# Optimization experiments

Hardware: AMD Instinct MI355X
Metric: run time of the kernel (lower is better)

The kernel has to match this reference:

```python
import jax, jax.numpy as jnp
from jax import lax
import numpy as np


def conv2d(x, w, pad):
    # x: NCHW, w: OIHW
    return lax.conv_general_dilated(x, w, (1, 1), [(pad, pad), (pad, pad)],
                                    dimension_numbers=("NCHW", "OIHW", "NCHW"))


def make_dct_dict(num_atoms, num_dims):
    i = np.arange(num_atoms)[:, None].astype(np.float64)
    n = np.arange(num_dims)[None, :].astype(np.float64)
    w = np.cos((2.0 * n + 1.0) * i * (np.pi / (2.0 * num_dims)))
    w = w / np.linalg.norm(w, axis=1, keepdims=True)
    return jnp.asarray(w.T, dtype=jnp.float32)  # [num_dims, num_atoms]


def setup_inputs() -> dict:
    key = jax.random.key(0)
    B, C, H, W = 8, 64, 64, 64      # C = num_dims
    A = 256                          # num_atoms
    ks = jax.random.split(key, 10)
    s = 0.05
    Dict = make_dct_dict(A, C)       # [C, A]
    L = jnp.sum(Dict ** 2)           # ||Dict||_F^2 (scalar parameter)
    return {
        "x": jax.random.normal(ks[0], (B, C, H, W), jnp.float32),
        "conv_w": jax.random.normal(ks[1], (A, C, 3, 3), jnp.float32) * s,
        "conv_b": jax.random.normal(ks[2], (A,), jnp.float32) * s,
        "res1_w1": jax.random.normal(ks[3], (A // 2, A, 3, 3), jnp.float32) * s,
        "res1_w2": jax.random.normal(ks[4], (A, A // 2, 1, 1), jnp.float32) * s,
        "res2_w1": jax.random.normal(ks[5], (A // 2, A, 3, 3), jnp.float32) * s,
        "res2_w2": jax.random.normal(ks[6], (A, A // 2, 1, 1), jnp.float32) * s,
        "ca_w1": jax.random.normal(ks[7], (A // 16, A), jnp.float32) * s,  # Linear(A, A//16)
        "ca_w2": jax.random.normal(ks[8], (A, A // 16), jnp.float32) * s,  # Linear(A//16, A)
        "sa_w": jax.random.normal(ks[9], (1, 2, 3, 3), jnp.float32) * s,
        "Dict": Dict,
        "L": L,
        "num_iters": 16,
    }


def reference(x, conv_w, conv_b, res1_w1, res1_w2, res2_w1, res2_w2,
              ca_w1, ca_w2, sa_w, Dict, L, num_iters):
    def res_block(h, w1, w2):
        t = conv2d(jax.nn.relu(h), w1, 1)
        t = conv2d(jax.nn.relu(t), w2, 0)
        return h + t

    l = conv2d(x, conv_w, 1) + conv_b[None, :, None, None]
    l = res_block(l, res1_w1, res1_w2)
    l = res_block(l, res2_w1, res2_w2)

    # CBAM: channel attention (shared MLP on avg/max pooled features)
    avg = jnp.mean(l, axis=(2, 3))  # [B, A]
    mx = jnp.max(l, axis=(2, 3))
    fc = lambda v: jax.nn.relu(v @ ca_w1.T) @ ca_w2.T
    l = l * jax.nn.sigmoid(fc(avg) + fc(mx))[:, :, None, None]
    # CBAM: spatial attention
    s2 = jnp.concatenate([jnp.mean(l, axis=1, keepdims=True),
                          jnp.max(l, axis=1, keepdims=True)], axis=1)  # [B,2,H,W]
    l = l * jax.nn.sigmoid(conv2d(s2, sa_w, 1))

    lam = jnp.transpose(l / L, (0, 2, 3, 1))   # [B,H,W,A] per-position thresholds
    xp = jnp.transpose(x, (0, 2, 3, 1))        # [B,H,W,C]

    A = Dict.shape[1]
    S = (jnp.eye(A, dtype=Dict.dtype) - (Dict.T @ Dict) / L).T  # [A,A]
    y = xp @ Dict                               # [B,H,W,A]
    yL = y / L

    soft = lambda v: jnp.sign(v) * jnp.maximum(jnp.abs(v) - lam, 0.0)

    z0 = soft(y)

    def step(z, _):
        return soft(z @ S + yL), None

    z, _ = lax.scan(step, z0, None, length=num_iters)
    x_recon = z @ Dict.T                        # [B,H,W,C]

    return (jnp.transpose(z, (0, 3, 1, 2)),
            jnp.transpose(x_recon, (0, 3, 1, 2)),
            Dict)
```

## Files before the change

### kernel.cpp

```cpp
#include <hip/hip_runtime.h>
#include <hip/hip_bf16.h>

typedef __attribute__((ext_vector_type(8))) short short8v;
typedef __attribute__((ext_vector_type(4))) short short4v;
typedef __attribute__((ext_vector_type(4))) float float4v;

__device__ __forceinline__ unsigned short f2bu(float v){
  __hip_bfloat16 h = __float2bfloat16(v);
  union { __hip_bfloat16 h; unsigned short u; } cv; cv.h = h; return cv.u;
}

__device__ __forceinline__ float softt(float v, float lam){
  float t = fabsf(v) - lam;
  float sg = (v > 0.f) ? 1.f : ((v < 0.f) ? -1.f : 0.f);
  return (t > 0.f) ? sg * t : 0.f;
}

__global__ void k_Lin(const float* __restrict__ Lsrc, float* __restrict__ Lb){
  Lb[0] = Lsrc[0];
}

__global__ void k_gram(const float* __restrict__ D, unsigned short* __restrict__ Gb){
  int j = blockIdx.x, a = threadIdx.x;
  float acc = 0.f;
  for (int c = 0; c < 64; ++c)
    acc += D[c*256 + j] * D[c*256 + a];
  Gb[j*256 + a] = f2bu(acc);
}

__global__ void k_transpD(const float* __restrict__ D, float* __restrict__ DT,
                          unsigned short* __restrict__ DTb){
  int gid = blockIdx.x * 256 + threadIdx.x;
  if (gid < 16384) {
    int a = gid >> 6, c = gid & 63;
    float v = D[c*256 + a];
    DT[gid] = v;
    DTb[gid] = f2bu(v);
  }
}

__global__ void k_castw(const float* __restrict__ w, unsigned short* __restrict__ wb,
                        int n){
  int gid = blockIdx.x * 256 + threadIdx.x;
  if (gid < n) wb[gid] = f2bu(w[gid]);
}

__global__ void k_permw3(const float* __restrict__ w, unsigned short* __restrict__ wb,
                         int logI, int n){
  int gid = blockIdx.x * 256 + threadIdx.x;
  if (gid >= n) return;
  int I = 1 << logI;
  int i = gid & (I - 1);
  int t = gid >> logI;
  int o = t / 9;
  int r = t - o * 9;
  wb[gid] = f2bu(w[((o << logI) + i) * 9 + r]);
}

template<int KS, int CIN, bool BIAS, bool RES, bool WF32, bool WBF>
__global__ __launch_bounds__(256) void k_conv(
    const unsigned short* __restrict__ in, const unsigned short* __restrict__ wb,
    const float* __restrict__ bias, const float* res, float* outf,
    unsigned short* __restrict__ outb, int Cout)
{
  constexpr int NCH  = CIN / 32;
  constexpr int LNCH = (NCH == 2) ? 1 : (NCH == 4 ? 2 : 3);
  constexpr int K    = KS * KS * CIN;

  __shared__ unsigned short Asb[32][40];
  __shared__ unsigned short Bsb[128][40];

  const int tid = threadIdx.x;
  int bx = blockIdx.x;
  { const int cpx = gridDim.x >> 3; bx = (bx & 7) * cpx + (bx >> 3); }
  const int m0  = bx * 32;
  const int n0  = blockIdx.y * 128;
  const int b   = m0 >> 12;
  const int hw0 = m0 & 4095;
  const int h   = hw0 >> 6;
  const int w0  = hw0 & 63;

  const int sm  = tid & 31;
  const int sq4 = tid >> 5;
  const int bn  = tid & 127;
  const int bq  = tid >> 7;

  const int w   = tid >> 6;
  const int ln  = tid & 63;
  const int q   = ln >> 4;
  const int l16 = ln & 15;

  float4v acc[2][2];
  #pragma unroll
  for (int nt = 0; nt < 2; ++nt)
    #pragma unroll
    for (int mt = 0; mt < 2; ++mt)
      acc[nt][mt] = (float4v){0.f, 0.f, 0.f, 0.f};

  int sA = 0, sB = NCH;
  if (KS == 3) { sA = (h == 0 ? 3 : 0) * NCH; sB = (h == 63 ? 6 : 9) * NCH; }

  short4v a_r;
  short8v b_r0, b_r1;

  auto pref = [&](int s){
    const int r    = s >> LNCH;
    const int ccid = s & (NCH - 1);
    int hh = h, ww = w0 + sm;
    bool ok = true;
    if (KS == 3) {
      const int dh = r / 3 - 1;
      const int dw = r - (r / 3) * 3 - 1;
      hh += dh; ww += dw;
      ok = ((unsigned)ww < 64u);
    }
    a_r = (short4v){0, 0, 0, 0};
    if (ok) {
      const unsigned short* ap = in +
          (((size_t)(b * CIN + ccid * 32 + sq4 * 4)) << 12) + (hh << 6) + ww;
      #pragma unroll
      for (int j = 0; j < 4; ++j)
        a_r[j] = (short)ap[(size_t)j << 12];
    }
    const unsigned short* bp = wb + (size_t)(n0 + bn) * K + s * 32 + bq * 16;
    b_r0 = *(const short8v*)(bp);
    b_r1 = *(const short8v*)(bp + 8);
  };

  pref(sA);
  for (int s = sA; s < sB; ) {
    *(short4v*)(&Asb[sm][sq4 * 4])      = a_r;
    *(short8v*)(&Bsb[bn][bq * 16])      = b_r0;
    *(short8v*)(&Bsb[bn][bq * 16 + 8])  = b_r1;
    __syncthreads();
    const int sn = s + 1;
    if (sn < sB) pref(sn);
    short8v Af[2];
    #pragma unroll
    for (int mt = 0; mt < 2; ++mt)
      Af[mt] = *(const short8v*)(&Asb[mt * 16 + l16][q * 8]);
    #pragma unroll
    for (int nt = 0; nt < 2; ++nt) {
      short8v Bf = *(const short8v*)(&Bsb[w * 32 + nt * 16 + l16][q * 8]);
      #pragma unroll
      for (int mt = 0; mt < 2; ++mt)
        acc[nt][mt] = __builtin_amdgcn_mfma_f32_16x16x32_bf16(
            Af[mt], Bf, acc[nt][mt], 0, 0, 0);
    }
    __syncthreads();
    s = sn;
  }

  #pragma unroll
  for (int nt = 0; nt < 2; ++nt) {
    const int n = n0 + w * 32 + nt * 16 + l16;
    float bv = 0.f;
    if (BIAS) bv = bias[n];
    #pragma unroll
    for (int mt = 0; mt < 2; ++mt) {
      const size_t base = (((size_t)(b * Cout + n)) << 12) + hw0 + mt * 16 + q * 4;
      float o[4];
      #pragma unroll
      for (int r2 = 0; r2 < 4; ++r2) o[r2] = acc[nt][mt][r2] + bv;
      if (RES) {
        float4 r4 = *(const float4*)(res + base);
        o[0] += r4.x; o[1] += r4.y; o[2] += r4.z; o[3] += r4.w;
      }
      if (WF32) {
        float4 o4; o4.x = o[0]; o4.y = o[1]; o4.z = o[2]; o4.w = o[3];
        *(float4*)(outf + base) = o4;
      }
      if (WBF) {
        short4v s4;
        #pragma unroll
        for (int r2 = 0; r2 < 4; ++r2) s4[r2] = (short)f2bu(fmaxf(o[r2], 0.f));
        *(short4v*)(outb + base) = s4;
      }
    }
  }
}

__global__ void k_pool(const float* __restrict__ l, float* __restrict__ avg,
                       float* __restrict__ mx){
  int b = blockIdx.y, a = blockIdx.x, tid = threadIdx.x;
  const float* p = l + ((size_t)(b * 256 + a) << 12);
  float s = 0.f, m = -1e30f;
  for (int i = tid; i < 4096; i += 256) { float v = p[i]; s += v; m = fmaxf(m, v); }
  __shared__ float ss[256], sm[256];
  ss[tid] = s; sm[tid] = m; __syncthreads();
  for (int o = 128; o > 0; o >>= 1) {
    if (tid < o) { ss[tid] += ss[tid+o]; sm[tid] = fmaxf(sm[tid], sm[tid+o]); }
    __syncthreads();
  }
  if (tid == 0) { avg[b*256+a] = ss[0] * (1.f/4096.f); mx[b*256+a] = sm[0]; }
}

__global__ void k_ca(const float* __restrict__ avg, const float* __restrict__ mx,
                     const float* __restrict__ w1, const float* __restrict__ w2,
                     float* __restrict__ cscale){
  int b = blockIdx.x, tid = threadIdx.x;
  __shared__ float h[16];
  if (tid < 16) {
    float sa = 0.f, sm = 0.f;
    for (int a = 0; a < 256; ++a) {
      float w = w1[tid*256 + a];
      sa += avg[b*256 + a] * w;
      sm += mx[b*256 + a] * w;
    }
    h[tid] = fmaxf(sa, 0.f) + fmaxf(sm, 0.f);
  }
  __syncthreads();
  float s = 0.f;
  for (int j = 0; j < 16; ++j) s += h[j] * w2[tid*16 + j];
  cscale[b*256 + tid] = 1.f / (1.f + __expf(-s));
}

__global__ void k_s2(const float* __restrict__ l, const float* __restrict__ cscale,
                     float* __restrict__ s2){
  int b = blockIdx.y;
  int hw = blockIdx.x * 256 + threadIdx.x;
  const float* p  = l + (((size_t)b * 256) << 12) + hw;
  const float* cs = cscale + b * 256;
  float s = 0.f, m = -1e30f;
  for (int a = 0; a < 256; ++a) {
    float v = p[(size_t)a << 12] * cs[a];
    s += v; m = fmaxf(m, v);
  }
  s2[((b*2) << 12) + hw]   = s * (1.f/256.f);
  s2[((b*2+1) << 12) + hw] = m;
}

__global__ void k_sa(const float* __restrict__ s2, const float* __restrict__ w,
                     float* __restrict__ sa){
  int b = blockIdx.y;
  int hw = blockIdx.x * 256 + threadIdx.x;
  int h = hw >> 6, ww = hw & 63;
  float acc = 0.f;
  for (int ch = 0; ch < 2; ++ch)
    for (int dh = -1; dh <= 1; ++dh)
      for (int dw = -1; dw <= 1; ++dw) {
        int hh = h + dh, wc = ww + dw;
        if ((unsigned)hh < 64u && (unsigned)wc < 64u)
          acc += s2[((b*2+ch) << 12) + (hh << 6) + wc] * w[ch*9 + (dh+1)*3 + (dw+1)];
      }
  sa[(b << 12) + hw] = 1.f / (1.f + __expf(-acc));
}

#define XTS 80

__device__ __forceinline__ int zswz(int row, int col){
  return row * 256 + ((((col >> 3) ^ (row & 7)) << 3) | (col & 7));
}

__global__ __launch_bounds__(512, 2) void k_lista(
    const float* __restrict__ x,
    const unsigned short* __restrict__ DTb,
    const unsigned short* __restrict__ Gb,
    const float* __restrict__ lmap, const float* __restrict__ csc,
    const float* __restrict__ sav, const float* __restrict__ Lb,
    float* __restrict__ zout)
{
  __shared__ unsigned short xTb[32][XTS];
  __shared__ unsigned short zbuf[2][32 * 256];

  const int tid = threadIdx.x;
  const int m0  = blockIdx.x * 32;
  const int b   = m0 >> 12;
  const int hw0 = m0 & 4095;
  const float invL = 1.0f / Lb[0];

  {
    const int i  = tid & 31;
    const int c0 = tid >> 5;
    #pragma unroll
    for (int cc = 0; cc < 4; ++cc) {
      int c = c0 + cc * 16;
      xTb[i][c] = f2bu(x[((b * 64 + c) << 12) + hw0 + i]);
    }
  }
  __syncthreads();

  const int w   = tid >> 6;
  const int ln  = tid & 63;
  const int q   = ln >> 4;
  const int l16 = ln & 15;

  float z[4][4], yl[4][4], lamr[4][4];

  #pragma unroll
  for (int ct = 0; ct < 2; ++ct) {
    const int col = w * 32 + ct * 16 + l16;
    const short8v B0 = *(const short8v*)(DTb + col * 64 + q * 8);
    const short8v B1 = *(const short8v*)(DTb + col * 64 + 32 + q * 8);
    const float cscv = csc[b * 256 + col];
    #pragma unroll
    for (int rt = 0; rt < 2; ++rt) {
      float4v a = {0.f, 0.f, 0.f, 0.f};
      const short8v A0 = *(const short8v*)(&xTb[rt * 16 + l16][q * 8]);
      const short8v A1 = *(const short8v*)(&xTb[rt * 16 + l16][32 + q * 8]);
      a = __builtin_amdgcn_mfma_f32_16x16x32_bf16(A0, B0, a, 0, 0, 0);
      a = __builtin_amdgcn_mfma_f32_16x16x32_bf16(A1, B1, a, 0, 0, 0);
      const int t = ct * 2 + rt;
      #pragma unroll
      for (int r = 0; r < 4; ++r) {
        const int row = rt * 16 + q * 4 + r;
        const float lv = lmap[(((size_t)(b * 256 + col)) << 12) + hw0 + row];
        const float sv = sav[(b << 12) + hw0 + row];
        const float lm = ((lv * cscv) * sv) * invL;
        const float yv = a[r];
        lamr[t][r] = lm;
        yl[t][r]   = yv * invL;
        const float z0 = softt(yv, lm);
        z[t][r] = z0;
        zbuf[0][zswz(row, col)] = f2bu(z0);
      }
    }
  }

  short8v Bg[2][8];
  #pragma unroll
  for (int ct = 0; ct < 2; ++ct)
    #pragma unroll
    for (int ks = 0; ks < 8; ++ks)
      Bg[ct][ks] = *(const short8v*)(
          Gb + (size_t)(w * 32 + ct * 16 + l16) * 256 + ks * 32 + q * 8);

  __syncthreads();

  const int rx = l16 & 7;
  int cur = 0;
  for (int it = 0; it < 16; ++it) {
    float4v acc[2][2];
    #pragma unroll
    for (int ct = 0; ct < 2; ++ct)
      #pragma unroll
      for (int rt = 0; rt < 2; ++rt)
        acc[ct][rt] = (float4v){0.f, 0.f, 0.f, 0.f};

    #pragma unroll
    for (int rt = 0; rt < 2; ++rt) {
      const unsigned short* zrow = &zbuf[cur][(rt * 16 + l16) * 256];
      #pragma unroll
      for (int ks = 0; ks < 8; ++ks) {
        const short8v A = *(const short8v*)(zrow + (((ks * 4 + q) ^ rx) << 3));
        acc[0][rt] = __builtin_amdgcn_mfma_f32_16x16x32_bf16(A, Bg[0][ks], acc[0][rt], 0, 0, 0);
        acc[1][rt] = __builtin_amdgcn_mfma_f32_16x16x32_bf16(A, Bg[1][ks], acc[1][rt], 0, 0, 0);
      }
    }
    #pragma unroll
    for (int ct = 0; ct < 2; ++ct) {
      const int col = w * 32 + ct * 16 + l16;
      #pragma unroll
      for (int rt = 0; rt < 2; ++rt) {
        const int t = ct * 2 + rt;
        #pragma unroll
        for (int r = 0; r < 4; ++r) {
          const int row = rt * 16 + q * 4 + r;
          const float nz = softt(z[t][r] + yl[t][r] - acc[ct][rt][r] * invL,
                                 lamr[t][r]);
          z[t][r] = nz;
          zbuf[cur ^ 1][zswz(row, col)] = f2bu(nz);
        }
      }
    }
    __syncthreads();
    cur ^= 1;
  }

  #pragma unroll
  for (int ct = 0; ct < 2; ++ct) {
    const int col = w * 32 + ct * 16 + l16;
    #pragma unroll
    for (int rt = 0; rt < 2; ++rt) {
      const int t = ct * 2 + rt;
      #pragma unroll
      for (int r = 0; r < 4; ++r) {
        const int row = rt * 16 + q * 4 + r;
        zout[(size_t)(m0 + row) * 256 + col] = z[t][r];
      }
    }
  }
}

__global__ __launch_bounds__(256) void k_recon_simple(
    const float* __restrict__ z, const float* __restrict__ DT,
    float* __restrict__ out1)
{
  __shared__ float zs[16][256];
  const int tid = threadIdx.x;
  const int r0  = blockIdx.x * 16;
  const int b   = r0 >> 12;
  const int hw0 = r0 & 4095;

  for (int idx = tid; idx < 4096; idx += 256) {
    int r = idx >> 8, k = idx & 255;
    zs[r][k] = z[(r0 + r) * 256 + k];
  }
  __syncthreads();

  const int c  = tid & 63;
  const int rg = tid >> 6;
  float acc[4] = {0.f, 0.f, 0.f, 0.f};
  for (int a = 0; a < 256; ++a) {
    float d = DT[a * 64 + c];
    #pragma unroll
    for (int i = 0; i < 4; ++i) acc[i] += zs[rg + 4*i][a] * d;
  }
  #pragma unroll
  for (int i = 0; i < 4; ++i) {
    int r = rg + 4*i;
    out1[((b * 64 + c) << 12) + hw0 + r] = acc[i];
  }
}

__global__ __launch_bounds__(256) void k_zout_t(const float* __restrict__ z,
                                                float* __restrict__ out0){
  __shared__ float zs[64][65];
  const int tid = threadIdx.x;
  const int hwt = blockIdx.x * 64;
  const int at  = blockIdx.y * 64;
  const int b   = blockIdx.z;
  const int j   = tid & 63;
  const int i0  = tid >> 6;
  #pragma unroll
  for (int k = 0; k < 16; ++k) {
    int i = i0 + k * 4;
    zs[i][j] = z[(size_t)(b * 4096 + hwt + i) * 256 + at + j];
  }
  __syncthreads();
  #pragma unroll
  for (int k = 0; k < 16; ++k) {
    int i = i0 + k * 4;
    out0[(((size_t)(b * 256 + at + i)) << 12) + hwt + j] = zs[j][i];
  }
}

__global__ void k_dictout_f32(const float* __restrict__ D, float* __restrict__ out2){
  int i = blockIdx.x * 256 + threadIdx.x;
  if (i < 16384) out2[i] = D[i];
}

extern "C" void kernel_launch(void* const* d_in, const int* in_sizes, int n_in,
                              void* d_out, int out_size, void* d_ws, size_t ws_size,
                              hipStream_t stream)
{
  (void)in_sizes; (void)n_in; (void)out_size; (void)ws_size;

  const float* x    = (const float*)d_in[0];
  const float* cw   = (const float*)d_in[1];
  const float* cb   = (const float*)d_in[2];
  const float* r1w1 = (const float*)d_in[3];
  const float* r1w2 = (const float*)d_in[4];
  const float* r2w1 = (const float*)d_in[5];
  const float* r2w2 = (const float*)d_in[6];
  const float* caw1 = (const float*)d_in[7];
  const float* caw2 = (const float*)d_in[8];
  const float* saw  = (const float*)d_in[9];
  const float* D    = (const float*)d_in[10];
  const float* Lsrc = (const float*)d_in[11];

  float* p = (float*)d_ws;
  float* DT   = p; p += 16384;
  float* Lb   = p; p += 8;
  unsigned short* Gb  = (unsigned short*)p; p += 32768;
  unsigned short* DTb = (unsigned short*)p; p += 8192;
  unsigned short* cwb   = (unsigned short*)p; p += 73728;
  unsigned short* r1w1b = (unsigned short*)p; p += 147456;
  unsigned short* r1w2b = (unsigned short*)p; p += 16384;
  unsigned short* r2w1b = (unsigned short*)p; p += 147456;
  unsigned short* r2w2b = (unsigned short*)p; p += 16384;
  float* avg  = p; p += 2048;
  float* mx   = p; p += 2048;
  float* csc  = p; p += 2048;
  float* s2   = p; p += 65536;
  float* sa   = p; p += 32768;
  float* l    = p; p += 8388608;
  float* scr  = p; p += 8388608;
  float* zt   = p; p += 8388608;
  float* z    = zt;

  unsigned short* xb = (unsigned short*)scr;
  unsigned short* lb = (unsigned short*)(scr + 1048576);
  unsigned short* tb = (unsigned short*)(scr + 1048576 + 4194304);

  float* out0 = (float*)d_out;
  float* out1 = out0 + (size_t)8*256*4096;
  float* out2 = out1 + (size_t)8*64*4096;

  dim3 b256(256);

  k_Lin<<<dim3(1), dim3(1), 0, stream>>>(Lsrc, Lb);
  k_gram<<<dim3(256), b256, 0, stream>>>(D, Gb);
  k_transpD<<<dim3(64), b256, 0, stream>>>(D, DT, DTb);
  k_permw3<<<dim3(576),  b256, 0, stream>>>(cw,   cwb,   6, 147456);
  k_permw3<<<dim3(1152), b256, 0, stream>>>(r1w1, r1w1b, 8, 294912);
  k_castw <<<dim3(128),  b256, 0, stream>>>(r1w2, r1w2b, 32768);
  k_permw3<<<dim3(1152), b256, 0, stream>>>(r2w1, r2w1b, 8, 294912);
  k_castw <<<dim3(128),  b256, 0, stream>>>(r2w2, r2w2b, 32768);
  k_castw <<<dim3(8192), b256, 0, stream>>>(x, xb, 2097152);

  k_conv<3,  64, true,  false, true,  true ><<<dim3(1024, 2), b256, 0, stream>>>(
      xb, cwb, cb, (const float*)nullptr, l, lb, 256);
  k_conv<3, 256, false, false, false, true ><<<dim3(1024, 1), b256, 0, stream>>>(
      lb, r1w1b, (const float*)nullptr, (const float*)nullptr, (float*)nullptr, tb, 128);
  k_conv<1, 128, false, true,  true,  true ><<<dim3(1024, 2), b256, 0, stream>>>(
      tb, r1w2b, (const float*)nullptr, l, l, lb, 256);
  k_conv<3, 256, false, false, false, true ><<<dim3(1024, 1), b256, 0, stream>>>(
      lb, r2w1b, (const float*)nullptr, (const float*)nullptr, (float*)nullptr, tb, 128);
  k_conv<1, 128, false, true,  true,  false><<<dim3(1024, 2), b256, 0, stream>>>(
      tb, r2w2b, (const float*)nullptr, l, l, (unsigned short*)nullptr, 256);

  k_pool<<<dim3(256, 8), b256, 0, stream>>>(l, avg, mx);
  k_ca<<<dim3(8), b256, 0, stream>>>(avg, mx, caw1, caw2, csc);
  k_s2<<<dim3(16, 8), b256, 0, stream>>>(l, csc, s2);
  k_sa<<<dim3(16, 8), b256, 0, stream>>>(s2, saw, sa);

  k_lista<<<dim3(1024), dim3(512), 0, stream>>>(x, DTb, Gb, l, csc, sa, Lb, z);

  k_recon_simple<<<dim3(2048), b256, 0, stream>>>(z, DT, out1);
  k_zout_t<<<dim3(64, 4, 8), b256, 0, stream>>>(z, out0);
  k_dictout_f32<<<dim3(64), b256, 0, stream>>>(D, out2);
}
```

Baseline: 579.8 us.

## Enlarge conv M-tile to 64 pixels and transpose LISTA MFMA operand roles

The conv kernel now covers 64 output pixels per block instead of 32, with 4 M-subtiles per wave. This halves the grid and reuses each loaded weight tile across twice as many pixels, at the cost of more accumulator registers. The LISTA kernel swaps MFMA operands so the Gram matrix is the A operand and z is B. That lets each lane hold 4 consecutive atoms, so z is written to LDS as packed short4 stores and to global memory as float4 stores instead of scalar ones. The soft-threshold is also rewritten branch-free with copysign, and the occupancy hint on LISTA is dropped.

After: 489.1 us. -15.7%, faster.

```diff
diff --git a/kernel.cpp b/kernel.cpp
--- a/kernel.cpp
+++ b/kernel.cpp
@@ -11,9 +11,9 @@
 }
 
 __device__ __forceinline__ float softt(float v, float lam){
-  float t = fabsf(v) - lam;
-  float sg = (v > 0.f) ? 1.f : ((v < 0.f) ? -1.f : 0.f);
-  return (t > 0.f) ? sg * t : 0.f;
+  float t = fmaxf(fabsf(v) - lam, 0.f);
+  float r = copysignf(t, v);
+  return (v == 0.f) ? 0.f : r;
 }
 
 __global__ void k_Lin(const float* __restrict__ Lsrc, float* __restrict__ Lb){
@@ -67,21 +67,21 @@
   constexpr int LNCH = (NCH == 2) ? 1 : (NCH == 4 ? 2 : 3);
   constexpr int K    = KS * KS * CIN;
 
-  __shared__ unsigned short Asb[32][40];
+  __shared__ unsigned short Asb[64][40];
   __shared__ unsigned short Bsb[128][40];
 
   const int tid = threadIdx.x;
   int bx = blockIdx.x;
   { const int cpx = gridDim.x >> 3; bx = (bx & 7) * cpx + (bx >> 3); }
-  const int m0  = bx * 32;
+  const int m0  = bx * 64;
   const int n0  = blockIdx.y * 128;
   const int b   = m0 >> 12;
   const int hw0 = m0 & 4095;
   const int h   = hw0 >> 6;
   const int w0  = hw0 & 63;
 
-  const int sm  = tid & 31;
-  const int sq4 = tid >> 5;
+  const int sm  = tid & 63;
+  const int sq8 = tid >> 6;
   const int bn  = tid & 127;
   const int bq  = tid >> 7;
 
@@ -90,17 +90,17 @@
   const int q   = ln >> 4;
   const int l16 = ln & 15;
 
-  float4v acc[2][2];
+  float4v acc[2][4];
   #pragma unroll
   for (int nt = 0; nt < 2; ++nt)
     #pragma unroll
-    for (int mt = 0; mt < 2; ++mt)
+    for (int mt = 0; mt < 4; ++mt)
       acc[nt][mt] = (float4v){0.f, 0.f, 0.f, 0.f};
 
   int sA = 0, sB = NCH;
   if (KS == 3) { sA = (h == 0 ? 3 : 0) * NCH; sB = (h == 63 ? 6 : 9) * NCH; }
 
-  short4v a_r;
+  short8v a_r;
   short8v b_r0, b_r1;
 
   auto pref = [&](int s){
@@ -114,12 +114,12 @@
       hh += dh; ww += dw;
       ok = ((unsigned)ww < 64u);
     }
-    a_r = (short4v){0, 0, 0, 0};
+    a_r = (short8v){0,0,0,0,0,0,0,0};
     if (ok) {
       const unsigned short* ap = in +
-          (((size_t)(b * CIN + ccid * 32 + sq4 * 4)) << 12) + (hh << 6) + ww;
-      #pragma unroll
-      for (int j = 0; j < 4; ++j)
+          (((size_t)(b * CIN + ccid * 32 + sq8 * 8)) << 12) + (hh << 6) + ww;
+      #pragma unroll
+      for (int j = 0; j < 8; ++j)
         a_r[j] = (short)ap[(size_t)j << 12];
     }
     const unsigned short* bp = wb + (size_t)(n0 + bn) * K + s * 32 + bq * 16;
@@ -129,21 +129,21 @@
 
   pref(sA);
   for (int s = sA; s < sB; ) {
-    *(short4v*)(&Asb[sm][sq4 * 4])      = a_r;
+    *(short8v*)(&Asb[sm][sq8 * 8])      = a_r;
     *(short8v*)(&Bsb[bn][bq * 16])      = b_r0;
     *(short8v*)(&Bsb[bn][bq * 16 + 8])  = b_r1;
     __syncthreads();
     const int sn = s + 1;
     if (sn < sB) pref(sn);
-    short8v Af[2];
-    #pragma unroll
-    for (int mt = 0; mt < 2; ++mt)
+    short8v Af[4];
+    #pragma unroll
+    for (int mt = 0; mt < 4; ++mt)
       Af[mt] = *(const short8v*)(&Asb[mt * 16 + l16][q * 8]);
     #pragma unroll
     for (int nt = 0; nt < 2; ++nt) {
       short8v Bf = *(const short8v*)(&Bsb[w * 32 + nt * 16 + l16][q * 8]);
       #pragma unroll
-      for (int mt = 0; mt < 2; ++mt)
+      for (int mt = 0; mt < 4; ++mt)
         acc[nt][mt] = __builtin_amdgcn_mfma_f32_16x16x32_bf16(
             Af[mt], Bf, acc[nt][mt], 0, 0, 0);
     }
@@ -157,7 +157,7 @@
     float bv = 0.f;
     if (BIAS) bv = bias[n];
     #pragma unroll
-    for (int mt = 0; mt < 2; ++mt) {
+    for (int mt = 0; mt < 4; ++mt) {
       const size_t base = (((size_t)(b * Cout + n)) << 12) + hw0 + mt * 16 + q * 4;
       float o[4];
       #pragma unroll
@@ -248,11 +248,7 @@
 
 #define XTS 80
 
-__device__ __forceinline__ int zswz(int row, int col){
-  return row * 256 + ((((col >> 3) ^ (row & 7)) << 3) | (col & 7));
-}
-
-__global__ __launch_bounds__(512, 2) void k_lista(
+__global__ __launch_bounds__(512) void k_lista(
     const float* __restrict__ x,
     const unsigned short* __restrict__ DTb,
     const unsigned short* __restrict__ Gb,
@@ -284,83 +280,87 @@
   const int ln  = tid & 63;
   const int q   = ln >> 4;
   const int l16 = ln & 15;
+  const int rx  = l16 & 7;
 
   float z[4][4], yl[4][4], lamr[4][4];
 
-  #pragma unroll
-  for (int ct = 0; ct < 2; ++ct) {
-    const int col = w * 32 + ct * 16 + l16;
-    const short8v B0 = *(const short8v*)(DTb + col * 64 + q * 8);
-    const short8v B1 = *(const short8v*)(DTb + col * 64 + 32 + q * 8);
-    const float cscv = csc[b * 256 + col];
-    #pragma unroll
-    for (int rt = 0; rt < 2; ++rt) {
+  short8v Sg[2][8];
+  #pragma unroll
+  for (int at = 0; at < 2; ++at)
+    #pragma unroll
+    for (int ks = 0; ks < 8; ++ks)
+      Sg[at][ks] = *(const short8v*)(
+          Gb + (size_t)(w * 32 + at * 16 + l16) * 256 + ks * 32 + q * 8);
+
+  #pragma unroll
+  for (int at = 0; at < 2; ++at) {
+    const short8v A0 = *(const short8v*)(DTb + (w*32 + at*16 + l16) * 64 + q * 8);
+    const short8v A1 = *(const short8v*)(DTb + (w*32 + at*16 + l16) * 64 + 32 + q * 8);
+    const int chunk = ((w * 4 + at * 2 + (q >> 1)) ^ rx);
+    #pragma unroll
+    for (int pt = 0; pt < 2; ++pt) {
       float4v a = {0.f, 0.f, 0.f, 0.f};
-      const short8v A0 = *(const short8v*)(&xTb[rt * 16 + l16][q * 8]);
-      const short8v A1 = *(const short8v*)(&xTb[rt * 16 + l16][32 + q * 8]);
+      const short8v B0 = *(const short8v*)(&xTb[pt * 16 + l16][q * 8]);
+      const short8v B1 = *(const short8v*)(&xTb[pt * 16 + l16][32 + q * 8]);
       a = __builtin_amdgcn_mfma_f32_16x16x32_bf16(A0, B0, a, 0, 0, 0);
       a = __builtin_amdgcn_mfma_f32_16x16x32_bf16(A1, B1, a, 0, 0, 0);
-      const int t = ct * 2 + rt;
+      const int t = at * 2 + pt;
+      const int p = pt * 16 + l16;
+      short4v pk;
       #pragma unroll
       for (int r = 0; r < 4; ++r) {
-        const int row = rt * 16 + q * 4 + r;
-        const float lv = lmap[(((size_t)(b * 256 + col)) << 12) + hw0 + row];
-        const float sv = sav[(b << 12) + hw0 + row];
-        const float lm = ((lv * cscv) * sv) * invL;
+        const int atom = w * 32 + at * 16 + q * 4 + r;
+        const float lv = lmap[(((size_t)(b * 256 + atom)) << 12) + hw0 + p];
+        const float sv = sav[(b << 12) + hw0 + p];
+        const float cv = csc[b * 256 + atom];
+        const float lm = ((lv * cv) * sv) * invL;
         const float yv = a[r];
         lamr[t][r] = lm;
         yl[t][r]   = yv * invL;
         const float z0 = softt(yv, lm);
         z[t][r] = z0;
-        zbuf[0][zswz(row, col)] = f2bu(z0);
-      }
-    }
-  }
-
-  short8v Bg[2][8];
-  #pragma unroll
-  for (int ct = 0; ct < 2; ++ct)
-    #pragma unroll
-    for (int ks = 0; ks < 8; ++ks)
-      Bg[ct][ks] = *(const short8v*)(
-          Gb + (size_t)(w * 32 + ct * 16 + l16) * 256 + ks * 32 + q * 8);
-
+        pk[r] = (short)f2bu(z0);
+      }
+      *(short4v*)(&zbuf[0][p * 256 + (chunk << 3) + (q & 1) * 4]) = pk;
+    }
+  }
   __syncthreads();
 
-  const int rx = l16 & 7;
   int cur = 0;
   for (int it = 0; it < 16; ++it) {
     float4v acc[2][2];
     #pragma unroll
-    for (int ct = 0; ct < 2; ++ct)
-      #pragma unroll
-      for (int rt = 0; rt < 2; ++rt)
-        acc[ct][rt] = (float4v){0.f, 0.f, 0.f, 0.f};
-
-    #pragma unroll
-    for (int rt = 0; rt < 2; ++rt) {
-      const unsigned short* zrow = &zbuf[cur][(rt * 16 + l16) * 256];
+    for (int at = 0; at < 2; ++at)
+      #pragma unroll
+      for (int pt = 0; pt < 2; ++pt)
+        acc[at][pt] = (float4v){0.f, 0.f, 0.f, 0.f};
+
+    #pragma unroll
+    for (int pt = 0; pt < 2; ++pt) {
+      const unsigned short* zrow = &zbuf[cur][(pt * 16 + l16) * 256];
       #pragma unroll
       for (int ks = 0; ks < 8; ++ks) {
-        const short8v A = *(const short8v*)(zrow + (((ks * 4 + q) ^ rx) << 3));
-        acc[0][rt] = __builtin_amdgcn_mfma_f32_16x16x32_bf16(A, Bg[0][ks], acc[0][rt], 0, 0, 0);
-        acc[1][rt] = __builtin_amdgcn_mfma_f32_16x16x32_bf16(A, Bg[1][ks], acc[1][rt], 0, 0, 0);
-      }
-    }
-    #pragma unroll
-    for (int ct = 0; ct < 2; ++ct) {
-      const int col = w * 32 + ct * 16 + l16;
-      #pragma unroll
-      for (int rt = 0; rt < 2; ++rt) {
-        const int t = ct * 2 + rt;
+        const short8v B = *(const short8v*)(zrow + (((ks * 4 + q) ^ rx) << 3));
+        acc[0][pt] = __builtin_amdgcn_mfma_f32_16x16x32_bf16(Sg[0][ks], B, acc[0][pt], 0, 0, 0);
+        acc[1][pt] = __builtin_amdgcn_mfma_f32_16x16x32_bf16(Sg[1][ks], B, acc[1][pt], 0, 0, 0);
+      }
+    }
+    #pragma unroll
+    for (int at = 0; at < 2; ++at) {
+      const int chunk = ((w * 4 + at * 2 + (q >> 1)) ^ rx);
+      #pragma unroll
+      for (int pt = 0; pt < 2; ++pt) {
+        const int t = at * 2 + pt;
+        const int p = pt * 16 + l16;
+        short4v pk;
         #pragma unroll
         for (int r = 0; r < 4; ++r) {
-          const int row = rt * 16 + q * 4 + r;
-          const float nz = softt(z[t][r] + yl[t][r] - acc[ct][rt][r] * invL,
+          const float nz = softt(z[t][r] + yl[t][r] - acc[at][pt][r] * invL,
                                  lamr[t][r]);
           z[t][r] = nz;
-          zbuf[cur ^ 1][zswz(row, col)] = f2bu(nz);
+          pk[r] = (short)f2bu(nz);
         }
+        *(short4v*)(&zbuf[cur ^ 1][p * 256 + (chunk << 3) + (q & 1) * 4]) = pk;
       }
     }
     __syncthreads();
@@ -368,16 +368,14 @@
   }
 
   #pragma unroll
-  for (int ct = 0; ct < 2; ++ct) {
-    const int col = w * 32 + ct * 16 + l16;
-    #pragma unroll
-    for (int rt = 0; rt < 2; ++rt) {
-      const int t = ct * 2 + rt;
-      #pragma unroll
-      for (int r = 0; r < 4; ++r) {
-        const int row = rt * 16 + q * 4 + r;
-        zout[(size_t)(m0 + row) * 256 + col] = z[t][r];
-      }
+  for (int at = 0; at < 2; ++at) {
+    #pragma unroll
+    for (int pt = 0; pt < 2; ++pt) {
+      const int t = at * 2 + pt;
+      const int p = pt * 16 + l16;
+      float4 o;
+      o.x = z[t][0]; o.y = z[t][1]; o.z = z[t][2]; o.w = z[t][3];
+      *(float4*)(&zout[(size_t)(m0 + p) * 256 + w * 32 + at * 16 + q * 4]) = o;
     }
   }
 }
@@ -499,15 +497,15 @@
   k_castw <<<dim3(128),  b256, 0, stream>>>(r2w2, r2w2b, 32768);
   k_castw <<<dim3(8192), b256, 0, stream>>>(x, xb, 2097152);
 
-  k_conv<3,  64, true,  false, true,  true ><<<dim3(1024, 2), b256, 0, stream>>>(
+  k_conv<3,  64, true,  false, true,  true ><<<dim3(512, 2), b256, 0, stream>>>(
       xb, cwb, cb, (const float*)nullptr, l, lb, 256);
-  k_conv<3, 256, false, false, false, true ><<<dim3(1024, 1), b256, 0, stream>>>(
+  k_conv<3, 256, false, false, false, true ><<<dim3(512, 1), b256, 0, stream>>>(
       lb, r1w1b, (const float*)nullptr, (const float*)nullptr, (float*)nullptr, tb, 128);
-  k_conv<1, 128, false, true,  true,  true ><<<dim3(1024, 2), b256, 0, stream>>>(
+  k_conv<1, 128, false, true,  true,  true ><<<dim3(512, 2), b256, 0, stream>>>(
       tb, r1w2b, (const float*)nullptr, l, l, lb, 256);
-  k_conv<3, 256, false, false, false, true ><<<dim3(1024, 1), b256, 0, stream>>>(
+  k_conv<3, 256, false, false, false, true ><<<dim3(512, 1), b256, 0, stream>>>(
       lb, r2w1b, (const float*)nullptr, (const float*)nullptr, (float*)nullptr, tb, 128);
-  k_conv<1, 128, false, true,  true,  false><<<dim3(1024, 2), b256, 0, stream>>>(
+  k_conv<1, 128, false, true,  true,  false><<<dim3(512, 2), b256, 0, stream>>>(
       tb, r2w2b, (const float*)nullptr, l, l, (unsigned short*)nullptr, 256);
 
   k_pool<<<dim3(256, 8), b256, 0, stream>>>(l, avg, mx);
```
